# Optimization experiments

Measured on AMD Instinct MI355X. Metric: run time of the kernel, lower is better.

Reference implementation:

```python
import jax, jax.numpy as jnp
import numpy as np

N_NODES = 100000
N_EDGES = 3200000
D_FEAT = 128
HIDDEN = 16
N_CLASSES = 7


def gcn_conv(x, edge_index, edge_weight, W, b, n_nodes):
    h = x @ W  # dense projection first (Fout small)
    src, dst = edge_index[0], edge_index[1]
    # add self-loops with weight 1
    loop = jnp.arange(n_nodes, dtype=edge_index.dtype)
    src_a = jnp.concatenate([src, loop])
    dst_a = jnp.concatenate([dst, loop])
    ew_a = jnp.concatenate([edge_weight, jnp.ones((n_nodes,), dtype=x.dtype)])
    deg = jax.ops.segment_sum(ew_a, dst_a, num_segments=n_nodes)
    dinv = jnp.where(deg > 0, jax.lax.rsqrt(deg), 0.0)
    norm = dinv[src_a] * ew_a * dinv[dst_a]  # [E+N]
    msg = h[src_a] * norm[:, None]  # gather + scale
    out = jax.ops.segment_sum(msg, dst_a, num_segments=n_nodes)
    return out + b


def setup_inputs() -> dict:
    key = jax.random.key(0)
    k = jax.random.split(key, 8)
    x = jax.random.normal(k[0], (N_NODES, D_FEAT), dtype=jnp.float32)
    edge_index = jax.random.randint(k[1], (2, N_EDGES), 0, N_NODES, dtype=jnp.int64)
    edge_weight = jax.random.uniform(k[2], (N_EDGES,), dtype=jnp.float32)
    s1 = 1.0 / np.sqrt(D_FEAT)
    s2 = 1.0 / np.sqrt(HIDDEN)
    W1 = jax.random.uniform(k[3], (D_FEAT, HIDDEN), jnp.float32, -s1, s1)
    b1 = jnp.zeros((HIDDEN,), jnp.float32)
    W2 = jax.random.uniform(k[4], (HIDDEN, N_CLASSES), jnp.float32, -s2, s2)
    b2 = jnp.zeros((N_CLASSES,), jnp.float32)
    return {"x": x, "edge_index": edge_index, "edge_weight": edge_weight,
            "W1": W1, "b1": b1, "W2": W2, "b2": b2}


def reference(x, edge_index, edge_weight, W1, b1, W2, b2):
    h = jax.nn.relu(gcn_conv(x, edge_index, edge_weight, W1, b1, N_NODES))
    out = gcn_conv(h, edge_index, edge_weight, W2, b2, N_NODES)
    return jax.nn.log_softmax(out, axis=1)
```

## Files before the change

kernel.cpp:

```cpp
#include <hip/hip_runtime.h>
#include <hip/hip_fp16.h>
#include <math.h>

constexpr int NN = 100000;
constexpr int NE = 3200000;
constexpr int DF = 128;
constexpr int NH = 16;
constexpr int NC = 7;

constexpr int BN    = 256;
constexpr int NB    = (NN + BN - 1) / BN;
constexpr int CAP   = 9216;
constexpr int CHUNK = 4096;
constexpr int AB    = (NE + CHUNK - 1) / CHUNK;
constexpr int EPT   = CHUNK / 1024;
constexpr int SPT   = (CAP + 1023) / 1024;

constexpr float QS   = 32767.0f;
constexpr float QINV = 1.0f / 32767.0f;

typedef _Float16 half8 __attribute__((ext_vector_type(8)));
typedef float    f32x4 __attribute__((ext_vector_type(4)));

__global__ void k_zero(int* __restrict__ gcur) {
    int t = blockIdx.x * blockDim.x + threadIdx.x;
    if (t < NB) gcur[t] = 0;
}

__global__ void __launch_bounds__(1024)
k_append(const int* __restrict__ src,
         const int* __restrict__ dst,
         const float* __restrict__ w,
         int* __restrict__ gcur,
         uint2* __restrict__ ebuf) {
    __shared__ int hist[NB];
    __shared__ int cscan[512];
    __shared__ int basev[NB];
    __shared__ uint2 staged[CHUNK];
    __shared__ unsigned short sbkt[CHUNK];
    for (int i = threadIdx.x; i < NB; i += 1024) hist[i] = 0;
    __syncthreads();
    int e0 = blockIdx.x * CHUNK;
    unsigned slo[EPT], sw[EPT];
    int sbr[EPT];
#pragma unroll
    for (int k = 0; k < EPT; ++k) {
        int e = e0 + (int)threadIdx.x + k * 1024;
        sbr[k] = -1;
        if (e < NE) {
            int d = __builtin_nontemporal_load(dst + e);
            int b = d >> 8;
            int r = atomicAdd(&hist[b], 1);
            slo[k] = ((unsigned)(d & (BN - 1)) << 17) |
                     (unsigned)__builtin_nontemporal_load(src + e);
            sw[k]  = __float_as_uint(__builtin_nontemporal_load(w + e));
            sbr[k] = (b << 13) | r;
        }
    }
    __syncthreads();
    {
        int v0 = (threadIdx.x < NB) ? hist[threadIdx.x] : 0;
        if (threadIdx.x < 512) cscan[threadIdx.x] = v0;
        __syncthreads();
        for (int off = 1; off < 512; off <<= 1) {
            int v = (threadIdx.x < 512 && threadIdx.x >= off) ? cscan[threadIdx.x - off] : 0;
            __syncthreads();
            if (threadIdx.x < 512) cscan[threadIdx.x] += v;
            __syncthreads();
        }
    }
    if (threadIdx.x < NB) {
        int c = hist[threadIdx.x];
        basev[threadIdx.x] = (c > 0) ? atomicAdd(&gcur[threadIdx.x], c) : 0;
    }
    __syncthreads();
#pragma unroll
    for (int k = 0; k < EPT; ++k) {
        if (sbr[k] >= 0) {
            int b = sbr[k] >> 13;
            int idx = (cscan[b] - hist[b]) + (sbr[k] & 0x1FFF);
            uint2 v; v.x = slo[k]; v.y = sw[k];
            staged[idx] = v;
            sbkt[idx] = (unsigned short)b;
        }
    }
    __syncthreads();
    int total = min(CHUNK, NE - e0);
    for (int i = threadIdx.x; i < total; i += 1024) {
        int b = sbkt[i];
        int st = cscan[b] - hist[b];
        int pos = basev[b] + (i - st);
        if (pos < CAP) ebuf[(size_t)b * CAP + pos] = staged[i];
    }
}

__global__ void __launch_bounds__(1024)
k_sort(const int* __restrict__ gcur,
       uint2* __restrict__ ebuf,
       int* __restrict__ rs,
       int* __restrict__ rc,
       float* __restrict__ dinv) {
    __shared__ int cursor[BN];
    __shared__ int scanS[BN];
    __shared__ int startEx[BN];
    __shared__ unsigned sorted[CAP];
    int b = blockIdx.x;
    int tid = threadIdx.x;
    int cnt = min(gcur[b], CAP);
    const uint2* eb = ebuf + (size_t)b * CAP;
    if (tid < BN) cursor[tid] = 0;
    __syncthreads();
    unsigned sval[SPT];
    int sdr[SPT];
#pragma unroll
    for (int k = 0; k < SPT; ++k) {
        int i = tid + k * 1024;
        sdr[k] = -1;
        if (i < cnt) {
            uint2 v = eb[i];
            int dl = (v.x >> 17) & (BN - 1);
            unsigned q = (unsigned)(__uint_as_float(v.y) * QS + 0.5f);
            int r = atomicAdd(&cursor[dl], 1);
            sval[k] = (v.x & 0x1FFFF) | (q << 17);
            sdr[k] = (dl << 14) | r;
        }
    }
    __syncthreads();
    if (tid < BN) scanS[tid] = cursor[tid];
    __syncthreads();
    for (int off = 1; off < BN; off <<= 1) {
        int v = (tid < BN && tid >= off) ? scanS[tid - off] : 0;
        __syncthreads();
        if (tid < BN) scanS[tid] += v;
        __syncthreads();
    }
    if (tid < BN) {
        int ex = scanS[tid] - cursor[tid];
        startEx[tid] = ex;
        int n = b * BN + tid;
        if (n < NN) { rs[n] = b * CAP * 2 + ex; rc[n] = cursor[tid]; }
    }
    __syncthreads();
#pragma unroll
    for (int k = 0; k < SPT; ++k) {
        if (sdr[k] >= 0)
            sorted[startEx[sdr[k] >> 14] + (sdr[k] & 0x3FFF)] = sval[k];
    }
    __syncthreads();
    unsigned* eb32 = (unsigned*)ebuf + (size_t)b * CAP * 2;
    for (int i = tid; i < cnt; i += 1024) eb32[i] = sorted[i];
    if (tid < BN) {
        int n = b * BN + tid;
        if (n < NN) {
            float s = 1.0f;
            int s0 = startEx[tid], c = cursor[tid];
            for (int i = 0; i < c; ++i) s += (float)(sorted[s0 + i] >> 17) * QINV;
            dinv[n] = rsqrtf(s);
        }
    }
}

__global__ void __launch_bounds__(256)
k_proj1(const float* __restrict__ x,
        const float* __restrict__ W1,
        const float* __restrict__ dinv,
        __half* __restrict__ h1p) {
    int wave = threadIdx.x >> 6;
    int lane = threadIdx.x & 63;
    int tile = blockIdx.x * 4 + wave;
    if (tile * 16 >= NN) return;
    int m    = lane & 15;
    int quad = lane >> 4;
    half8 bfrag[4];
#pragma unroll
    for (int kc = 0; kc < 4; ++kc)
#pragma unroll
        for (int j = 0; j < 8; ++j)
            bfrag[kc][j] = (_Float16)W1[(kc * 32 + quad * 8 + j) * NH + m];
    int base = tile * 16;
    const float* xr = x + (size_t)(base + m) * DF + quad * 8;
    f32x4 acc = {0.f, 0.f, 0.f, 0.f};
#pragma unroll
    for (int kc = 0; kc < 4; ++kc) {
        const float4* p = (const float4*)(xr + kc * 32);
        float4 u0 = p[0];
        float4 u1 = p[1];
        half8 afrag;
        afrag[0] = (_Float16)u0.x; afrag[1] = (_Float16)u0.y;
        afrag[2] = (_Float16)u0.z; afrag[3] = (_Float16)u0.w;
        afrag[4] = (_Float16)u1.x; afrag[5] = (_Float16)u1.y;
        afrag[6] = (_Float16)u1.z; afrag[7] = (_Float16)u1.w;
        acc = __builtin_amdgcn_mfma_f32_16x16x32_f16(afrag, bfrag[kc], acc, 0, 0, 0);
    }
    float4 d4 = *(const float4*)(dinv + base + quad * 4);
#pragma unroll
    for (int reg = 0; reg < 4; ++reg) {
        float dd = (reg == 0) ? d4.x : (reg == 1) ? d4.y : (reg == 2) ? d4.z : d4.w;
        int row = quad * 4 + reg;
        h1p[(size_t)(base + row) * 16 + m] = __float2half(acc[reg] * dd);
    }
}

__global__ void __launch_bounds__(1024)
k_agg1p(const int* __restrict__ rs,
        const int* __restrict__ rc,
        const unsigned* __restrict__ cbuf,
        const __half* __restrict__ h1p,
        const float* __restrict__ dinv,
        const float* __restrict__ b1,
        const float* __restrict__ W2,
        __half* __restrict__ h2p) {
    const __half2* hp = (const __half2*)h1p;
    int t = blockIdx.x * 1024 + threadIdx.x;
    int n = t >> 3;
    int f2 = t & 7;
    if (n >= NN) return;
    float2 g0 = __half22float2(hp[n * 8 + f2]);
    float ax = g0.x, ay = g0.y;
    int s0 = rs[n], c = rc[n];
    int i = 0;
    for (; i + 1 < c; i += 2) {
        unsigned e0 = cbuf[s0 + i];
        unsigned e1 = cbuf[s0 + i + 1];
        float2 v0 = __half22float2(hp[(e0 & 0x1FFFF) * 8 + f2]);
        float2 v1 = __half22float2(hp[(e1 & 0x1FFFF) * 8 + f2]);
        float w0 = (float)(e0 >> 17) * QINV;
        float w1 = (float)(e1 >> 17) * QINV;
        ax += w0 * v0.x + w1 * v1.x;
        ay += w0 * v0.y + w1 * v1.y;
    }
    if (i < c) {
        unsigned e0 = cbuf[s0 + i];
        float2 v0 = __half22float2(hp[(e0 & 0x1FFFF) * 8 + f2]);
        float w0 = (float)(e0 >> 17) * QINV;
        ax += w0 * v0.x;
        ay += w0 * v0.y;
    }
    float di = dinv[n];
    float hr0 = fmaxf(di * ax + b1[2 * f2], 0.0f);
    float hr1 = fmaxf(di * ay + b1[2 * f2 + 1], 0.0f);
    float p[NC];
#pragma unroll
    for (int cc = 0; cc < NC; ++cc)
        p[cc] = hr0 * W2[(2 * f2) * NC + cc] + hr1 * W2[(2 * f2 + 1) * NC + cc];
#pragma unroll
    for (int mask = 1; mask < 8; mask <<= 1) {
#pragma unroll
        for (int cc = 0; cc < NC; ++cc)
            p[cc] += __shfl_xor(p[cc], mask, 8);
    }
    float tv = 0.0f;
#pragma unroll
    for (int cc = 0; cc < NC; ++cc)
        if (f2 == cc) tv = p[cc];
    h2p[n * 8 + f2] = __float2half(di * tv);
}

__global__ void __launch_bounds__(1024)
k_agg2_lsm(const int* __restrict__ rs,
           const int* __restrict__ rc,
           const unsigned* __restrict__ cbuf,
           const __half* __restrict__ h2p,
           const float* __restrict__ dinv,
           const float* __restrict__ b2,
           float* __restrict__ out) {
    const __half2* hp = (const __half2*)h2p;
    int t = blockIdx.x * 1024 + threadIdx.x;
    int n = t >> 2;
    int c2 = t & 3;
    if (n >= NN) return;
    float2 g0 = __half22float2(hp[n * 4 + c2]);
    float ax = g0.x, ay = g0.y;
    int s0 = rs[n], c = rc[n];
    int i = 0;
    for (; i + 1 < c; i += 2) {
        unsigned e0 = cbuf[s0 + i];
        unsigned e1 = cbuf[s0 + i + 1];
        float2 v0 = __half22float2(hp[(e0 & 0x1FFFF) * 4 + c2]);
        float2 v1 = __half22float2(hp[(e1 & 0x1FFFF) * 4 + c2]);
        float w0 = (float)(e0 >> 17) * QINV;
        float w1 = (float)(e1 >> 17) * QINV;
        ax += w0 * v0.x + w1 * v1.x;
        ay += w0 * v0.y + w1 * v1.y;
    }
    if (i < c) {
        unsigned e0 = cbuf[s0 + i];
        float2 v0 = __half22float2(hp[(e0 & 0x1FFFF) * 4 + c2]);
        float w0 = (float)(e0 >> 17) * QINV;
        ax += w0 * v0.x;
        ay += w0 * v0.y;
    }
    float di = dinv[n];
    float va = di * ax + b2[2 * c2];
    float vb = (c2 < 3) ? (di * ay + b2[2 * c2 + 1]) : -1e30f;
    float m = fmaxf(va, vb);
#pragma unroll
    for (int mask = 1; mask < 4; mask <<= 1)
        m = fmaxf(m, __shfl_xor(m, mask, 4));
    float s = __expf(va - m) + ((c2 < 3) ? __expf(vb - m) : 0.0f);
#pragma unroll
    for (int mask = 1; mask < 4; mask <<= 1)
        s += __shfl_xor(s, mask, 4);
    float lse = m + __logf(s);
    out[n * NC + 2 * c2] = va - lse;
    if (c2 < 3) out[n * NC + 2 * c2 + 1] = vb - lse;
}

extern "C" void kernel_launch(void* const* d_in, const int* in_sizes, int n_in,
                              void* d_out, int out_size, void* d_ws, size_t ws_size,
                              hipStream_t stream) {
    const float* x  = (const float*)d_in[0];
    const int*   ei = (const int*)d_in[1];
    const float* ew = (const float*)d_in[2];
    const float* W1 = (const float*)d_in[3];
    const float* b1 = (const float*)d_in[4];
    const float* W2 = (const float*)d_in[5];
    const float* b2 = (const float*)d_in[6];
    float* out = (float*)d_out;

    const int* srcp = ei;
    const int* dstp = ei + NE;

    float*  ws   = (float*)d_ws;
    float*  dinv = ws;
    __half* h1p  = (__half*)(ws + 100352);
    __half* h2p  = (__half*)(ws + 900352);
    int*    gcur = (int*)(ws + 1300352);
    int*    rs   = (int*)(ws + 1301376);
    int*    rc   = (int*)(ws + 1401728);
    uint2*  ebuf = (uint2*)(ws + 1502080);
    const unsigned* cbuf = (const unsigned*)ebuf;

    auto cdiv = [](long long a, long long b) { return (int)((a + b - 1) / b); };

    k_zero<<<1, 1024, 0, stream>>>(gcur);
    k_append<<<AB, 1024, 0, stream>>>(srcp, dstp, ew, gcur, ebuf);
    k_sort<<<NB, 1024, 0, stream>>>(gcur, ebuf, rs, rc, dinv);
    k_proj1<<<cdiv(NN, 64), 256, 0, stream>>>(x, W1, dinv, h1p);
    k_agg1p<<<cdiv((long long)NN * 8, 1024), 1024, 0, stream>>>(rs, rc, cbuf, h1p, dinv, b1, W2, h2p);
    k_agg2_lsm<<<cdiv((long long)NN * 4, 1024), 1024, 0, stream>>>(rs, rc, cbuf, h2p, dinv, b2, out);
}
```

Measured before the change: 226.0 us.

## Widen per-thread feature vectors in aggregation and parallelize degree sum across lanes

Both aggregation kernels now process four features per thread with 8-byte gathers instead of two features with 4-byte gathers. This halves the number of threads that re-read each node's edge list, cutting redundant index loads. The degree reduction in the sort kernel now uses four lanes per node with a shuffle reduction instead of one serial thread per node. Weight quantization moves into the append kernel. The wider threads lower thread-level parallelism and add per-thread register work, and the 16-bit weight field in the staged word still relies on the later shift.

```diff
diff --git a/kernel.cpp b/kernel.cpp
--- a/kernel.cpp
+++ b/kernel.cpp
@@ -53,7 +53,7 @@
             int r = atomicAdd(&hist[b], 1);
             slo[k] = ((unsigned)(d & (BN - 1)) << 17) |
                      (unsigned)__builtin_nontemporal_load(src + e);
-            sw[k]  = __float_as_uint(__builtin_nontemporal_load(w + e));
+            sw[k]  = (unsigned)(__builtin_nontemporal_load(w + e) * QS + 0.5f);
             sbr[k] = (b << 13) | r;
         }
     }
@@ -119,9 +119,8 @@
         if (i < cnt) {
             uint2 v = eb[i];
             int dl = (v.x >> 17) & (BN - 1);
-            unsigned q = (unsigned)(__uint_as_float(v.y) * QS + 0.5f);
             int r = atomicAdd(&cursor[dl], 1);
-            sval[k] = (v.x & 0x1FFFF) | (q << 17);
+            sval[k] = (v.x & 0x1FFFF) | (v.y << 17);
             sdr[k] = (dl << 14) | r;
         }
     }
@@ -149,13 +148,16 @@
     __syncthreads();
     unsigned* eb32 = (unsigned*)ebuf + (size_t)b * CAP * 2;
     for (int i = tid; i < cnt; i += 1024) eb32[i] = sorted[i];
-    if (tid < BN) {
-        int n = b * BN + tid;
-        if (n < NN) {
-            float s = 1.0f;
-            int s0 = startEx[tid], c = cursor[tid];
-            for (int i = 0; i < c; ++i) s += (float)(sorted[s0 + i] >> 17) * QINV;
-            dinv[n] = rsqrtf(s);
+    {
+        int node = tid >> 2, part = tid & 3;
+        float s = (part == 0) ? 1.0f : 0.0f;
+        int s0 = startEx[node], c = cursor[node];
+        for (int i = part; i < c; i += 4) s += (float)(sorted[s0 + i] >> 17) * QINV;
+        s += __shfl_xor(s, 1, 4);
+        s += __shfl_xor(s, 2, 4);
+        if (part == 0) {
+            int n = b * BN + node;
+            if (n < NN) dinv[n] = rsqrtf(s);
         }
     }
 }
@@ -210,50 +212,83 @@
         const float* __restrict__ b1,
         const float* __restrict__ W2,
         __half* __restrict__ h2p) {
-    const __half2* hp = (const __half2*)h1p;
+    const uint2* hp4 = (const uint2*)h1p;
     int t = blockIdx.x * 1024 + threadIdx.x;
-    int n = t >> 3;
-    int f2 = t & 7;
+    int n = t >> 2;
+    int f4 = t & 3;
     if (n >= NN) return;
-    float2 g0 = __half22float2(hp[n * 8 + f2]);
-    float ax = g0.x, ay = g0.y;
+    float a0, a1, a2, a3;
+    {
+        uint2 u = hp4[n * 4 + f4];
+        float2 lo = __half22float2(*(const __half2*)&u.x);
+        float2 hi = __half22float2(*(const __half2*)&u.y);
+        a0 = lo.x; a1 = lo.y; a2 = hi.x; a3 = hi.y;
+    }
     int s0 = rs[n], c = rc[n];
     int i = 0;
     for (; i + 1 < c; i += 2) {
         unsigned e0 = cbuf[s0 + i];
         unsigned e1 = cbuf[s0 + i + 1];
-        float2 v0 = __half22float2(hp[(e0 & 0x1FFFF) * 8 + f2]);
-        float2 v1 = __half22float2(hp[(e1 & 0x1FFFF) * 8 + f2]);
+        uint2 u0 = hp4[(e0 & 0x1FFFF) * 4 + f4];
+        uint2 u1 = hp4[(e1 & 0x1FFFF) * 4 + f4];
         float w0 = (float)(e0 >> 17) * QINV;
         float w1 = (float)(e1 >> 17) * QINV;
-        ax += w0 * v0.x + w1 * v1.x;
-        ay += w0 * v0.y + w1 * v1.y;
+        float2 l0 = __half22float2(*(const __half2*)&u0.x);
+        float2 h0 = __half22float2(*(const __half2*)&u0.y);
+        float2 l1 = __half22float2(*(const __half2*)&u1.x);
+        float2 h1v = __half22float2(*(const __half2*)&u1.y);
+        a0 += w0 * l0.x + w1 * l1.x;
+        a1 += w0 * l0.y + w1 * l1.y;
+        a2 += w0 * h0.x + w1 * h1v.x;
+        a3 += w0 * h0.y + w1 * h1v.y;
     }
     if (i < c) {
         unsigned e0 = cbuf[s0 + i];
-        float2 v0 = __half22float2(hp[(e0 & 0x1FFFF) * 8 + f2]);
+        uint2 u0 = hp4[(e0 & 0x1FFFF) * 4 + f4];
         float w0 = (float)(e0 >> 17) * QINV;
-        ax += w0 * v0.x;
-        ay += w0 * v0.y;
+        float2 l0 = __half22float2(*(const __half2*)&u0.x);
+        float2 h0 = __half22float2(*(const __half2*)&u0.y);
+        a0 += w0 * l0.x;
+        a1 += w0 * l0.y;
+        a2 += w0 * h0.x;
+        a3 += w0 * h0.y;
     }
     float di = dinv[n];
-    float hr0 = fmaxf(di * ax + b1[2 * f2], 0.0f);
-    float hr1 = fmaxf(di * ay + b1[2 * f2 + 1], 0.0f);
-    float p[NC];
-#pragma unroll
-    for (int cc = 0; cc < NC; ++cc)
-        p[cc] = hr0 * W2[(2 * f2) * NC + cc] + hr1 * W2[(2 * f2 + 1) * NC + cc];
-#pragma unroll
-    for (int mask = 1; mask < 8; mask <<= 1) {
-#pragma unroll
-        for (int cc = 0; cc < NC; ++cc)
-            p[cc] += __shfl_xor(p[cc], mask, 8);
-    }
-    float tv = 0.0f;
-#pragma unroll
-    for (int cc = 0; cc < NC; ++cc)
-        if (f2 == cc) tv = p[cc];
-    h2p[n * 8 + f2] = __float2half(di * tv);
+    int fb = 4 * f4;
+    float hr0 = fmaxf(di * a0 + b1[fb + 0], 0.0f);
+    float hr1 = fmaxf(di * a1 + b1[fb + 1], 0.0f);
+    float hr2 = fmaxf(di * a2 + b1[fb + 2], 0.0f);
+    float hr3 = fmaxf(di * a3 + b1[fb + 3], 0.0f);
+    float p0, p1, p2, p3, p4, p5, p6;
+    {
+        const float* w0r = W2 + (fb + 0) * NC;
+        const float* w1r = W2 + (fb + 1) * NC;
+        const float* w2r = W2 + (fb + 2) * NC;
+        const float* w3r = W2 + (fb + 3) * NC;
+        p0 = hr0 * w0r[0] + hr1 * w1r[0] + hr2 * w2r[0] + hr3 * w3r[0];
+        p1 = hr0 * w0r[1] + hr1 * w1r[1] + hr2 * w2r[1] + hr3 * w3r[1];
+        p2 = hr0 * w0r[2] + hr1 * w1r[2] + hr2 * w2r[2] + hr3 * w3r[2];
+        p3 = hr0 * w0r[3] + hr1 * w1r[3] + hr2 * w2r[3] + hr3 * w3r[3];
+        p4 = hr0 * w0r[4] + hr1 * w1r[4] + hr2 * w2r[4] + hr3 * w3r[4];
+        p5 = hr0 * w0r[5] + hr1 * w1r[5] + hr2 * w2r[5] + hr3 * w3r[5];
+        p6 = hr0 * w0r[6] + hr1 * w1r[6] + hr2 * w2r[6] + hr3 * w3r[6];
+    }
+#pragma unroll
+    for (int mask = 1; mask < 4; mask <<= 1) {
+        p0 += __shfl_xor(p0, mask, 4);
+        p1 += __shfl_xor(p1, mask, 4);
+        p2 += __shfl_xor(p2, mask, 4);
+        p3 += __shfl_xor(p3, mask, 4);
+        p4 += __shfl_xor(p4, mask, 4);
+        p5 += __shfl_xor(p5, mask, 4);
+        p6 += __shfl_xor(p6, mask, 4);
+    }
+    float pa = (f4 == 0) ? p0 : (f4 == 1) ? p2 : (f4 == 2) ? p4 : p6;
+    float pb = (f4 == 0) ? p1 : (f4 == 1) ? p3 : (f4 == 2) ? p5 : 0.0f;
+    __half2 hv;
+    hv.x = __float2half(di * pa);
+    hv.y = __float2half(di * pb);
+    ((__half2*)h2p)[n * 4 + f4] = hv;
 }
 
 __global__ void __launch_bounds__(1024)
@@ -264,46 +299,63 @@
            const float* __restrict__ dinv,
            const float* __restrict__ b2,
            float* __restrict__ out) {
-    const __half2* hp = (const __half2*)h2p;
+    const uint2* hp2 = (const uint2*)h2p;
     int t = blockIdx.x * 1024 + threadIdx.x;
-    int n = t >> 2;
-    int c2 = t & 3;
+    int n = t >> 1;
+    int c2 = t & 1;
     if (n >= NN) return;
-    float2 g0 = __half22float2(hp[n * 4 + c2]);
-    float ax = g0.x, ay = g0.y;
+    float a0, a1, a2, a3;
+    {
+        uint2 u = hp2[n * 2 + c2];
+        float2 lo = __half22float2(*(const __half2*)&u.x);
+        float2 hi = __half22float2(*(const __half2*)&u.y);
+        a0 = lo.x; a1 = lo.y; a2 = hi.x; a3 = hi.y;
+    }
     int s0 = rs[n], c = rc[n];
     int i = 0;
     for (; i + 1 < c; i += 2) {
         unsigned e0 = cbuf[s0 + i];
         unsigned e1 = cbuf[s0 + i + 1];
-        float2 v0 = __half22float2(hp[(e0 & 0x1FFFF) * 4 + c2]);
-        float2 v1 = __half22float2(hp[(e1 & 0x1FFFF) * 4 + c2]);
+        uint2 u0 = hp2[(e0 & 0x1FFFF) * 2 + c2];
+        uint2 u1 = hp2[(e1 & 0x1FFFF) * 2 + c2];
         float w0 = (float)(e0 >> 17) * QINV;
         float w1 = (float)(e1 >> 17) * QINV;
-        ax += w0 * v0.x + w1 * v1.x;
-        ay += w0 * v0.y + w1 * v1.y;
+        float2 l0 = __half22float2(*(const __half2*)&u0.x);
+        float2 h0 = __half22float2(*(const __half2*)&u0.y);
+        float2 l1 = __half22float2(*(const __half2*)&u1.x);
+        float2 h1v = __half22float2(*(const __half2*)&u1.y);
+        a0 += w0 * l0.x + w1 * l1.x;
+        a1 += w0 * l0.y + w1 * l1.y;
+        a2 += w0 * h0.x + w1 * h1v.x;
+        a3 += w0 * h0.y + w1 * h1v.y;
     }
     if (i < c) {
         unsigned e0 = cbuf[s0 + i];
-        float2 v0 = __half22float2(hp[(e0 & 0x1FFFF) * 4 + c2]);
+        uint2 u0 = hp2[(e0 & 0x1FFFF) * 2 + c2];
         float w0 = (float)(e0 >> 17) * QINV;
-        ax += w0 * v0.x;
-        ay += w0 * v0.y;
+        float2 l0 = __half22float2(*(const __half2*)&u0.x);
+        float2 h0 = __half22float2(*(const __half2*)&u0.y);
+        a0 += w0 * l0.x;
+        a1 += w0 * l0.y;
+        a2 += w0 * h0.x;
+        a3 += w0 * h0.y;
     }
     float di = dinv[n];
-    float va = di * ax + b2[2 * c2];
-    float vb = (c2 < 3) ? (di * ay + b2[2 * c2 + 1]) : -1e30f;
-    float m = fmaxf(va, vb);
-#pragma unroll
-    for (int mask = 1; mask < 4; mask <<= 1)
-        m = fmaxf(m, __shfl_xor(m, mask, 4));
-    float s = __expf(va - m) + ((c2 < 3) ? __expf(vb - m) : 0.0f);
-#pragma unroll
-    for (int mask = 1; mask < 4; mask <<= 1)
-        s += __shfl_xor(s, mask, 4);
+    int cb = 4 * c2;
+    float va0 = di * a0 + b2[cb + 0];
+    float va1 = di * a1 + b2[cb + 1];
+    float va2 = di * a2 + b2[cb + 2];
+    float va3 = (c2 == 0) ? (di * a3 + b2[3]) : -1e30f;
+    float m = fmaxf(fmaxf(va0, va1), fmaxf(va2, va3));
+    m = fmaxf(m, __shfl_xor(m, 1, 2));
+    float s = __expf(va0 - m) + __expf(va1 - m) + __expf(va2 - m) + __expf(va3 - m);
+    s += __shfl_xor(s, 1, 2);
     float lse = m + __logf(s);
-    out[n * NC + 2 * c2] = va - lse;
-    if (c2 < 3) out[n * NC + 2 * c2 + 1] = vb - lse;
+    int base = n * NC + cb;
+    out[base + 0] = va0 - lse;
+    out[base + 1] = va1 - lse;
+    out[base + 2] = va2 - lse;
+    if (c2 == 0) out[base + 3] = va3 - lse;
 }
 
 extern "C" void kernel_launch(void* const* d_in, const int* in_sizes, int n_in,
@@ -337,6 +389,6 @@
     k_append<<<AB, 1024, 0, stream>>>(srcp, dstp, ew, gcur, ebuf);
     k_sort<<<NB, 1024, 0, stream>>>(gcur, ebuf, rs, rc, dinv);
     k_proj1<<<cdiv(NN, 64), 256, 0, stream>>>(x, W1, dinv, h1p);
-    k_agg1p<<<cdiv((long long)NN * 8, 1024), 1024, 0, stream>>>(rs, rc, cbuf, h1p, dinv, b1, W2, h2p);
-    k_agg2_lsm<<<cdiv((long long)NN * 4, 1024), 1024, 0, stream>>>(rs, rc, cbuf, h2p, dinv, b2, out);
-}
+    k_agg1p<<<cdiv((long long)NN * 4, 1024), 1024, 0, stream>>>(rs, rc, cbuf, h1p, dinv, b1, W2, h2p);
+    k_agg2_lsm<<<cdiv((long long)NN * 2, 1024), 1024, 0, stream>>>(rs, rc, cbuf, h2p, dinv, b2, out);
+}
```

Measured after the change: 231.3 us. 2.3% more time.
